# Optimization experiments

Hardware: AMD Instinct MI355X
Metric: run time of the kernel (lower is better)

## Reference

```python
import jax, jax.numpy as jnp
import numpy as np

B, N, H, L, V = 512, 24, 512, 64, 1024   # trees, nodes/tree, hidden, latent, vocab
MAX_NB = 8
T = 2 * (N - 1)      # DFS trace length per tree (each edge down + up)
PAD = T * B          # zero-padding slot in the message buffer


def _build_indices():
    rng = np.random.default_rng(0)
    wid = np.zeros((T, B), np.int32)
    ywid = np.zeros((T, B), np.int32)
    dirs = np.zeros((T, B), np.int32)
    hni = np.full((T, B, MAX_NB), PAD, np.int32)
    oni = np.full((T, B, MAX_NB), PAD, np.int32)
    rwid = np.zeros((B,), np.int32)
    roni = np.full((B, MAX_NB), PAD, np.int32)
    for b in range(B):
        deg = [0] * N
        nbr = [[] for _ in range(N)]
        for i in range(1, N):
            cand = [j for j in range(i) if deg[j] < MAX_NB]
            p = int(rng.choice(cand))
            nbr[p].append(i); nbr[i].append(p); deg[p] += 1; deg[i] += 1
        wids = rng.integers(0, V, N)
        trace = []
        def dfs(x, fa):
            for y in nbr[x]:
                if y == fa:
                    continue
                trace.append((x, y, 1)); dfs(y, x); trace.append((y, x, 0))
        dfs(0, -1)
        hkey = {}
        built = [[] for _ in range(N)]  # neighbors rebuilt as messages arrive
        for t, (x, y, d) in enumerate(trace):
            hn = [hkey[(z, x)] for z in built[x] if z != y]
            on = [hkey[(z, x)] for z in built[x]]
            hni[t, b, :len(hn)] = hn
            oni[t, b, :len(on)] = on
            wid[t, b] = wids[x]; ywid[t, b] = wids[y]; dirs[t, b] = d
            hkey[(x, y)] = t * B + b
            built[y].append(x)
        rwid[b] = wids[0]
        ron = [hkey[(z, 0)] for z in built[0]]
        roni[b, :len(ron)] = ron
    return wid, ywid, dirs, hni, oni, rwid, roni


def setup_inputs() -> dict:
    wid, ywid, dirs, hni, oni, rwid, roni = _build_indices()
    key = jax.random.key(0)
    ks = jax.random.split(key, 12)
    def pm(k, shape, s=0.05):
        return (jax.random.normal(k, shape) * s).astype(jnp.float32)
    return {
        "mol_vec": pm(ks[0], (B, L), 1.0),
        "wid": jnp.asarray(wid), "y_wid": jnp.asarray(ywid), "dirs": jnp.asarray(dirs),
        "h_nei_ids": jnp.asarray(hni), "o_nei_ids": jnp.asarray(oni),
        "root_wid": jnp.asarray(rwid), "root_o_nei_ids": jnp.asarray(roni),
        "emb": pm(ks[1], (V, H)),
        "Wz": pm(ks[2], (2 * H, H)), "bz": jnp.zeros((H,), jnp.float32),
        "Wr": pm(ks[3], (H, H)), "br": jnp.zeros((H,), jnp.float32),
        "Ur": pm(ks[4], (H, H)),
        "Wh": pm(ks[5], (2 * H, H)), "bh": jnp.zeros((H,), jnp.float32),
        "W": pm(ks[6], (L + H, H)), "bW": jnp.zeros((H,), jnp.float32),
        "U": pm(ks[7], (2 * H + L, H)), "bU": jnp.zeros((H,), jnp.float32),
        "Wo": pm(ks[8], (H, V)), "bo": jnp.zeros((V,), jnp.float32),
        "Us": pm(ks[9], (H, 1)), "bs": jnp.zeros((1,), jnp.float32),
    }


def _forward(mol_vec, emb, Wz, bz, Wr, br, Ur, Wh, bh, W, bW, U, bU, Wo, bo, Us, bs,
             wid, y_wid, dirs, h_nei_ids, o_nei_ids, root_wid, root_o_nei_ids):
    def gru(x, h_nei):  # x:[B,H], h_nei:[B,MAX_NB,H] (zero-padded)
        sum_h = h_nei.sum(1)
        z = jax.nn.sigmoid(jnp.concatenate([x, sum_h], -1) @ Wz + bz)
        r = jax.nn.sigmoid((x @ Wr + br)[:, None, :] + jnp.einsum('bnh,hk->bnk', h_nei, Ur))
        sum_g = (r * h_nei).sum(1)
        h_tilde = jnp.tanh(jnp.concatenate([x, sum_g], -1) @ Wh + bh)
        return (1.0 - z) * sum_h + z * h_tilde

    hbuf0 = jnp.zeros((T * B + 1, H), jnp.float32)  # last row = zero padding
    def step(hbuf, xs):
        t, w_t, ids_t = xs
        new_h = gru(emb[w_t], hbuf[ids_t])
        return jax.lax.dynamic_update_slice(hbuf, new_h, (t * B, 0)), None
    hbuf, _ = jax.lax.scan(step, hbuf0, (jnp.arange(T), wid, h_nei_ids))

    all_new_h = hbuf[:T * B]                  # [T*B, H] messages in step order
    cur_o = hbuf[o_nei_ids].sum(2)            # [T, B, H]
    x_emb = emb[wid]                          # [T, B, H]
    mv_rep = jnp.broadcast_to(mol_vec, (T, B, L))

    # ---- stop (BCE-with-logits, sum / B) ----
    stop_rows = jnp.concatenate([x_emb, cur_o, mv_rep], -1).reshape(T * B, 2 * H + L)
    root_row = jnp.concatenate([emb[root_wid], hbuf[root_o_nei_ids].sum(1), mol_vec], -1)
    stop_rows = jnp.concatenate([stop_rows, root_row], 0)
    stop_tgt = jnp.concatenate([dirs.reshape(-1).astype(jnp.float32), jnp.zeros((B,), jnp.float32)])
    s = (jax.nn.relu(stop_rows @ U + bU) @ Us + bs)[:, 0]
    stop_loss = (jnp.maximum(s, 0.0) - s * stop_tgt + jnp.log1p(jnp.exp(-jnp.abs(s)))).sum() / B
    stop_acc = jnp.mean(jnp.where((s >= 0.5) == (stop_tgt > 0.5), 1.0, 0.0))

    # ---- word prediction (CE, sum / B); root targets use zero hidden ----
    pred_h = jnp.concatenate([jnp.zeros((B, H), jnp.float32), all_new_h], 0)
    pred_mv = jnp.concatenate([mol_vec, mv_rep.reshape(T * B, L)], 0)
    pred_tgt = jnp.concatenate([root_wid, y_wid.reshape(-1)])
    mask = jnp.concatenate([jnp.ones((B,), jnp.float32), dirs.reshape(-1).astype(jnp.float32)])
    logits = jax.nn.relu(jnp.concatenate([pred_h, pred_mv], -1) @ W + bW) @ Wo + bo
    ls = jax.nn.log_softmax(logits, -1)
    ce = -jnp.take_along_axis(ls, pred_tgt[:, None], 1)[:, 0]
    pred_loss = (ce * mask).sum() / B
    preds = jnp.argmax(logits, 1)
    pred_acc = (jnp.where(preds == pred_tgt, 1.0, 0.0) * mask).sum() / mask.sum()
    return pred_loss, stop_loss, pred_acc, stop_acc


def reference(mol_vec, wid, y_wid, dirs, h_nei_ids, o_nei_ids, root_wid, root_o_nei_ids,
              emb, Wz, bz, Wr, br, Ur, Wh, bh, W, bW, U, bU, Wo, bo, Us, bs):
    return _forward(mol_vec, emb, Wz, bz, Wr, br, Ur, Wh, bh, W, bW, U, bU, Wo, bo, Us, bs,
                    wid, y_wid, dirs, h_nei_ids, o_nei_ids, root_wid, root_o_nei_ids)
```

## Files before the change

### kernel.cpp

```cpp
#include <hip/hip_runtime.h>
#include <hip/hip_bf16.h>

typedef __hip_bfloat16 bf16;
typedef __attribute__((ext_vector_type(8))) short bf16x8;
typedef __attribute__((ext_vector_type(4))) float f32x4;

static constexpr int Bb = 512;
static constexpr int Hh = 512;
static constexpr int Ll = 64;
static constexpr int Vv = 1024;
static constexpr int MAXNB = 8;
static constexpr int Tt = 46;
static constexpr int TB = Tt * Bb;
static constexpr int PADID = TB;
static constexpr int NROWS = TB + Bb;
static constexpr int XPS = 3 * Hh;

static constexpr int KU  = 2 * Hh + Ll;
static constexpr int KUP = KU + 8;
static constexpr int KW  = Hh + Ll;
static constexpr int KWP = KW + 8;
static constexpr int HP  = Hh + 8;

static constexpr int NT_U  = Hh / 16;
static constexpr int NT_WO = Vv / 16;

__device__ __forceinline__ float b2f(bf16 v) { return __bfloat162float(v); }
__device__ __forceinline__ float sigm(float x) { return 1.f / (1.f + __expf(-x)); }
__device__ __forceinline__ float bfu(unsigned short u) {
  return __uint_as_float((unsigned)u << 16);
}
__device__ __forceinline__ unsigned short f2bfu(float x) {
  bf16 v = __float2bfloat16(x);
  return *(unsigned short*)&v;
}

template <bool F32>
__device__ __forceinline__ float ldv(const void* p, long i) {
  if (F32) return ((const float*)p)[i];
  return __bfloat162float(((const bf16*)p)[i]);
}

__global__ void detect_kernel(const unsigned short* __restrict__ embu,
                              int* __restrict__ flag) {
  const long n = (long)Vv * Hh;
  int bad = 0;
  for (long i = blockIdx.x * 256 + threadIdx.x; i < n; i += 256L * 64) {
    unsigned short u = embu[i];
    if ((u & 0x7F80u) == 0x7F80u) bad = 1;
  }
  if (bad) atomicOr(flag, 1);
}

template <bool F32>
__device__ void xproj_body(const void* emb, const void* Wz, const void* bz,
                           const void* Wr, const void* br, const void* Wh,
                           const void* bh, bf16* xproj, float* xe) {
  const int v = blockIdx.x, k = threadIdx.x;
  xe[k] = ldv<F32>(emb, (long)v * Hh + k);
  __syncthreads();
  float z = ldv<F32>(bz, k);
  float r = ldv<F32>(br, k);
  float h = ldv<F32>(bh, k);
  for (int i = 0; i < Hh; ++i) {
    float a = xe[i];
    z += a * ldv<F32>(Wz, (long)i * Hh + k);
    r += a * ldv<F32>(Wr, (long)i * Hh + k);
    h += a * ldv<F32>(Wh, (long)i * Hh + k);
  }
  bf16* xp = xproj + (long)v * XPS;
  xp[k]          = __float2bfloat16(z);
  xp[Hh + k]     = __float2bfloat16(r);
  xp[2 * Hh + k] = __float2bfloat16(h);
}

__global__ __launch_bounds__(512) void xproj_kernel(
    const void* emb, const void* Wz, const void* bz, const void* Wr,
    const void* br, const void* Wh, const void* bh, bf16* xproj,
    const int* __restrict__ flag) {
  __shared__ float xe[Hh];
  if (*flag)
    xproj_body<true>(emb, Wz, bz, Wr, br, Wh, bh, xproj, xe);
  else
    xproj_body<false>(emb, Wz, bz, Wr, br, Wh, bh, xproj, xe);
}

template <bool F32>
__device__ __forceinline__ void wtt_body(const void* src, bf16* dst, int K,
                                         int N, int NT, int ro, int tk0,
                                         int tn0, unsigned short (*tile)[65]) {
  const int tid = threadIdx.x;
  const int ln = tid & 63;
  const int gr = tid >> 6;
  for (int kk = gr; kk < 64; kk += 4) {
    const int k = tk0 + kk, n = tn0 + ln;
    tile[ln][kk] = f2bfu(ldv<F32>(src, (long)(ro + k) * N + n));
  }
  __syncthreads();
  for (int nn = gr; nn < 64; nn += 4) {
    const int n = tn0 + nn, k = tk0 + ln;
    const long off = ((long)(k >> 5) * NT + (n >> 4)) * 512 +
                     ((k & 31) >> 3) * 128 + (n & 15) * 8 + (k & 7);
    dst[off] = *(bf16*)&tile[nn][ln];
  }
}

__global__ __launch_bounds__(256) void wt_kernel(
    const void* W, const void* U, const void* Wo, const void* Wz,
    const void* Ur, const void* Wh, bf16* wtW, bf16* wtU, bf16* wtWo,
    bf16* wgZ, bf16* wgR, bf16* wgH2, const int* __restrict__ flag) {
  __shared__ unsigned short tile[64][65];
  int b = blockIdx.x;
  const void* src; bf16* dst; int K, N, NT, ro, tk, tn;
  if (b < 72) {
    src = W; dst = wtW; K = KW; N = Hh; NT = NT_U; ro = 0; tk = b / 8; tn = b % 8;
  } else if (b < 208) {
    b -= 72; src = U; dst = wtU; K = KU; N = Hh; NT = NT_U; ro = 0; tk = b / 8; tn = b % 8;
  } else if (b < 336) {
    b -= 208; src = Wo; dst = wtWo; K = Hh; N = Vv; NT = NT_WO; ro = 0; tk = b / 16; tn = b % 16;
  } else if (b < 400) {
    b -= 336; src = Wz; dst = wgZ; K = Hh; N = Hh; NT = NT_U; ro = Hh; tk = b / 8; tn = b % 8;
  } else if (b < 464) {
    b -= 400; src = Ur; dst = wgR; K = Hh; N = Hh; NT = NT_U; ro = 0; tk = b / 8; tn = b % 8;
  } else {
    b -= 464; src = Wh; dst = wgH2; K = Hh; N = Hh; NT = NT_U; ro = Hh; tk = b / 8; tn = b % 8;
  }
  if (*flag) wtt_body<true>(src, dst, K, N, NT, ro, tk * 64, tn * 64, tile);
  else       wtt_body<false>(src, dst, K, N, NT, ro, tk * 64, tn * 64, tile);
}

__device__ __forceinline__ int gru_prep(int t, int b0, const int* hni,
                                        int* cid, int* rowf, int* nvs) {
  const int k = threadIdx.x;
  if (k < 2 * MAXNB)
    cid[k] = hni[((long)t * Bb + b0 + (k >> 3)) * MAXNB + (k & 7)];
  __syncthreads();
  if (k == 0) {
    int n0 = 0; while (n0 < MAXNB && cid[n0] != PADID) ++n0;
    int n1 = 0; while (n1 < MAXNB && cid[MAXNB + n1] != PADID) ++n1;
    for (int j = 0; j < n1; ++j) cid[n0 + j] = cid[MAXNB + j];
    for (int p = 0; p < n0 + n1; ++p) rowf[p] = (p >= n0) ? 1 : 0;
    nvs[0] = n0; nvs[1] = n1;
  }
  __syncthreads();
  return nvs[0] + nvs[1];
}

template <bool ABF, int S>
__device__ __forceinline__ void mfma_gemv(const bf16* __restrict__ Wt,
                                          const void* __restrict__ Abase,
                                          float* __restrict__ red,
                                          int wv, int l) {
  const int arow = l & 15;
  const int kofs = (l >> 4) * 8;
  f32x4 acc[4];
#pragma unroll
  for (int f = 0; f < 4; ++f) acc[f] = (f32x4){0.f, 0.f, 0.f, 0.f};

  for (int k0 = 0; k0 < Hh; k0 += 32) {
    unsigned short av[8] = {0, 0, 0, 0, 0, 0, 0, 0};
    if (arow < S) {
      if (ABF) {
        *(int4*)av = *(const int4*)((const bf16*)Abase + (long)arow * Hh +
                                    k0 + kofs);
      } else {
        const float* s = (const float*)Abase + (long)arow * Hh + k0 + kofs;
#pragma unroll
        for (int e = 0; e < 8; ++e) av[e] = f2bfu(s[e]);
      }
    }
    const bf16x8 a = *(const bf16x8*)av;
    const bf16* bkb = Wt + ((long)(k0 >> 5) * NT_U + wv * 4) * 512 + l * 8;
#pragma unroll
    for (int f = 0; f < 4; ++f) {
      const bf16x8 b = *(const bf16x8*)(bkb + f * 512);
      acc[f] = __builtin_amdgcn_mfma_f32_16x16x32_bf16(a, b, acc[f], 0, 0, 0);
    }
  }
#pragma unroll
  for (int f = 0; f < 4; ++f) {
    const int col = wv * 64 + f * 16 + (l & 15);
#pragma unroll
    for (int r = 0; r < 4; ++r) {
      const int row = (l >> 4) * 4 + r;
      if (row < S) red[row * Hh + col] = acc[f][r];
    }
  }
}

__global__ __launch_bounds__(512) void gru_step_xpb(
    int t, const int* __restrict__ wid, const int* __restrict__ hni,
    const bf16* __restrict__ xproj, const bf16* __restrict__ wgZ,
    const bf16* __restrict__ wgR, const bf16* __restrict__ wgH2,
    bf16* __restrict__ hbuf) {
  __shared__ float sh[2 * Hh];
  __shared__ float sg[2 * Hh];
  __shared__ __align__(16) unsigned short hnc[2 * MAXNB * Hh];
  __shared__ float red[4 * Hh];
  __shared__ int   cid[2 * MAXNB];
  __shared__ int   rowf[2 * MAXNB];
  __shared__ int   nvs[2];

  const int tid = threadIdx.x;
  const int k = tid;
  const int wv_ = tid >> 6;
  const int l = tid & 63;
  const int b0 = blockIdx.x * 2;
  const int P = gru_prep(t, b0, hni, cid, rowf, nvs);

  const int w0 = wid[t * Bb + b0];
  const int w1 = wid[t * Bb + b0 + 1];
  const bf16* xp0 = xproj + (long)w0 * XPS;
  const bf16* xp1 = xproj + (long)w1 * XPS;

  for (int p = wv_; p < P; p += 8) {
    const int4 d = *(const int4*)(hbuf + (long)cid[p] * Hh + 8 * l);
    *(int4*)(hnc + p * Hh + 8 * l) = d;
  }
  __syncthreads();

  float s0 = 0.f, s1 = 0.f;
  for (int p = 0; p < P; ++p) {
    const float hv = __bfloat162float(((const bf16*)hnc)[p * Hh + k]);
    if (rowf[p]) s1 += hv; else s0 += hv;
  }
  sh[k] = s0; sh[Hh + k] = s1;
  const float xz0 = b2f(xp0[k]),          xz1 = b2f(xp1[k]);
  const float xr0 = b2f(xp0[Hh + k]),     xr1 = b2f(xp1[Hh + k]);
  const float xh0 = b2f(xp0[2 * Hh + k]), xh1 = b2f(xp1[2 * Hh + k]);
  __syncthreads();

  mfma_gemv<false, 2>(wgZ, sh, red, wv_, l);
  __syncthreads();
  const float zp0 = xz0 + red[k];
  const float zp1 = xz1 + red[Hh + k];
  __syncthreads();

  float g0 = 0.f, g1 = 0.f;
  for (int c = 0; c < P; c += 4) {
    const int ns = (P - c >= 4) ? 4 : (P - c);
    const unsigned short* Ab = hnc + c * Hh;
    switch (ns) {
      case 1: mfma_gemv<true, 1>(wgR, Ab, red, wv_, l); break;
      case 2: mfma_gemv<true, 2>(wgR, Ab, red, wv_, l); break;
      case 3: mfma_gemv<true, 3>(wgR, Ab, red, wv_, l); break;
      default: mfma_gemv<true, 4>(wgR, Ab, red, wv_, l); break;
    }
    __syncthreads();
    for (int q = 0; q < ns; ++q) {
      const int p = c + q;
      const float rp = (rowf[p] ? xr1 : xr0) + red[q * Hh + k];
      const float cc =
          sigm(rp) * __bfloat162float(((const bf16*)hnc)[p * Hh + k]);
      if (rowf[p]) g1 += cc; else g0 += cc;
    }
    __syncthreads();
  }
  sg[k] = g0; sg[Hh + k] = g1;
  __syncthreads();

  mfma_gemv<false, 2>(wgH2, sg, red, wv_, l);
  __syncthreads();
  const float hp0 = xh0 + red[k];
  const float hp1 = xh1 + red[Hh + k];

  float z;
  z = sigm(zp0); const float o0 = (1.f - z) * s0 + z * tanhf(hp0);
  z = sigm(zp1); const float o1 = (1.f - z) * s1 + z * tanhf(hp1);
  hbuf[((long)t * Bb + b0) * Hh + k]     = __float2bfloat16(o0);
  hbuf[((long)t * Bb + b0 + 1) * Hh + k] = __float2bfloat16(o1);
}

template <bool F32, bool ABF, int S>
__device__ __forceinline__ void gemv_phase(const void* __restrict__ Wp,
                                           long wrow0,
                                           const void* __restrict__ Abase,
                                           float* __restrict__ red,
                                           int kg, int ch0) {
  float acc[S][4];
#pragma unroll
  for (int s = 0; s < S; ++s)
#pragma unroll
    for (int j = 0; j < 4; ++j) acc[s][j] = 0.f;
  const int i0 = kg * 128;
#pragma unroll 4
  for (int ii = 0; ii < 128; ++ii) {
    const int i = i0 + ii;
    float wv[4];
    if (F32) {
      const float4 f =
          *(const float4*)((const float*)Wp + (wrow0 + i) * (long)Hh + ch0);
      wv[0] = f.x; wv[1] = f.y; wv[2] = f.z; wv[3] = f.w;
    } else {
      const uint2 d =
          *(const uint2*)((const bf16*)Wp + (wrow0 + i) * (long)Hh + ch0);
      wv[0] = __uint_as_float(d.x << 16);
      wv[1] = __uint_as_float(d.x & 0xffff0000u);
      wv[2] = __uint_as_float(d.y << 16);
      wv[3] = __uint_as_float(d.y & 0xffff0000u);
    }
#pragma unroll
    for (int s = 0; s < S; ++s) {
      const float a = ABF
          ? __bfloat162float(((const bf16*)Abase)[s * Hh + i])
          : ((const float*)Abase)[s * Hh + i];
#pragma unroll
      for (int j = 0; j < 4; ++j) acc[s][j] += a * wv[j];
    }
  }
#pragma unroll
  for (int s = 0; s < S; ++s)
#pragma unroll
    for (int j = 0; j < 4; ++j)
      red[(kg * 4 + s) * Hh + ch0 + j] = acc[s][j];
}

template <bool F32>
__device__ void gru_body_xp(int t, const int* wid, const int* hni,
                            const bf16* xproj, const void* Wz, const void* Ur,
                            const void* Wh, bf16* hbuf, float* sh, float* sg,
                            unsigned short* hnc, float* red, int* cid,
                            int* rowf, int* nvs) {
  const int tid = threadIdx.x;
  const int k = tid;
  const int wv_ = tid >> 6;
  const int l = tid & 63;
  const int kg = wv_ >> 1;
  const int ch0 = (wv_ & 1) * 256 + l * 4;
  const int b0 = blockIdx.x * 2;
  const int P = gru_prep(t, b0, hni, cid, rowf, nvs);

  const int w0 = wid[t * Bb + b0];
  const int w1 = wid[t * Bb + b0 + 1];
  const bf16* xp0 = xproj + (long)w0 * XPS;
  const bf16* xp1 = xproj + (long)w1 * XPS;

  for (int p = wv_; p < P; p += 8) {
    const int4 d = *(const int4*)(hbuf + (long)cid[p] * Hh + 8 * l);
    *(int4*)(hnc + p * Hh + 8 * l) = d;
  }
  __syncthreads();

  float s0 = 0.f, s1 = 0.f;
  for (int p = 0; p < P; ++p) {
    const float hv = __bfloat162float(((const bf16*)hnc)[p * Hh + k]);
    if (rowf[p]) s1 += hv; else s0 += hv;
  }
  sh[k] = s0; sh[Hh + k] = s1;
  const float xz0 = b2f(xp0[k]),          xz1 = b2f(xp1[k]);
  const float xr0 = b2f(xp0[Hh + k]),     xr1 = b2f(xp1[Hh + k]);
  const float xh0 = b2f(xp0[2 * Hh + k]), xh1 = b2f(xp1[2 * Hh + k]);
  __syncthreads();

  gemv_phase<F32, false, 2>(Wz, Hh, sh, red, kg, ch0);
  __syncthreads();
  float zp0 = xz0, zp1 = xz1;
#pragma unroll
  for (int g = 0; g < 4; ++g) {
    zp0 += red[(g * 4 + 0) * Hh + k];
    zp1 += red[(g * 4 + 1) * Hh + k];
  }
  __syncthreads();

  float g0 = 0.f, g1 = 0.f;
  for (int c = 0; c < P; c += 4) {
    const int ns = (P - c >= 4) ? 4 : (P - c);
    const unsigned short* Ab = hnc + c * Hh;
    switch (ns) {
      case 1: gemv_phase<F32, true, 1>(Ur, 0, Ab, red, kg, ch0); break;
      case 2: gemv_phase<F32, true, 2>(Ur, 0, Ab, red, kg, ch0); break;
      case 3: gemv_phase<F32, true, 3>(Ur, 0, Ab, red, kg, ch0); break;
      default: gemv_phase<F32, true, 4>(Ur, 0, Ab, red, kg, ch0); break;
    }
    __syncthreads();
    for (int q = 0; q < ns; ++q) {
      const int p = c + q;
      float rp = rowf[p] ? xr1 : xr0;
#pragma unroll
      for (int g = 0; g < 4; ++g) rp += red[(g * 4 + q) * Hh + k];
      const float cc =
          sigm(rp) * __bfloat162float(((const bf16*)hnc)[p * Hh + k]);
      if (rowf[p]) g1 += cc; else g0 += cc;
    }
    __syncthreads();
  }
  sg[k] = g0; sg[Hh + k] = g1;
  __syncthreads();

  gemv_phase<F32, false, 2>(Wh, Hh, sg, red, kg, ch0);
  __syncthreads();
  float hp0 = xh0, hp1 = xh1;
#pragma unroll
  for (int g = 0; g < 4; ++g) {
    hp0 += red[(g * 4 + 0) * Hh + k];
    hp1 += red[(g * 4 + 1) * Hh + k];
  }

  float z;
  z = sigm(zp0); const float o0 = (1.f - z) * s0 + z * tanhf(hp0);
  z = sigm(zp1); const float o1 = (1.f - z) * s1 + z * tanhf(hp1);
  hbuf[((long)t * Bb + b0) * Hh + k]     = __float2bfloat16(o0);
  hbuf[((long)t * Bb + b0 + 1) * Hh + k] = __float2bfloat16(o1);
}

__global__ __launch_bounds__(512) void gru_step_xp(
    int t, const int* __restrict__ wid, const int* __restrict__ hni,
    const bf16* xproj, const void* Wz, const void* Ur, const void* Wh,
    bf16* hbuf, const int* __restrict__ flag) {
  __shared__ float sh[2 * Hh];
  __shared__ float sg[2 * Hh];
  __shared__ __align__(16) unsigned short hnc[2 * MAXNB * Hh];
  __shared__ float red[4 * 4 * Hh];
  __shared__ int   cid[2 * MAXNB];
  __shared__ int   rowf[2 * MAXNB];
  __shared__ int   nvs[2];
  if (*flag)
    gru_body_xp<true>(t, wid, hni, xproj, Wz, Ur, Wh, hbuf, sh, sg, hnc, red,
                      cid, rowf, nvs);
  else
    gru_body_xp<false>(t, wid, hni, xproj, Wz, Ur, Wh, hbuf, sh, sg, hnc, red,
                       cid, rowf, nvs);
}

template <bool F32, int P>
__device__ __forceinline__ void sumg(const void* Ur, int k, const float* hnc,
                                     float p0, float p1, const int* rowf,
                                     float& g0, float& g1) {
  float a[P];
#pragma unroll
  for (int p = 0; p < P; ++p) a[p] = rowf[p] ? p1 : p0;
  for (int i = 0; i < Hh; ++i) {
    float uv = ldv<F32>(Ur, (long)i * Hh + k);
#pragma unroll
    for (int p = 0; p < P; ++p) a[p] += hnc[p * Hh + i] * uv;
  }
#pragma unroll
  for (int p = 0; p < P; ++p) {
    float c = sigm(a[p]) * hnc[p * Hh + k];
    if (rowf[p]) g1 += c; else g0 += c;
  }
}

#define SUMG_SWITCH(F32V)                                                     \
  switch (P) {                                                                \
    case 1:  sumg<F32V, 1 >(Ur, k, hnc, p0, p1, rowf, g0, g1); break;         \
    case 2:  sumg<F32V, 2 >(Ur, k, hnc, p0, p1, rowf, g0, g1); break;         \
    case 3:  sumg<F32V, 3 >(Ur, k, hnc, p0, p1, rowf, g0, g1); break;         \
    case 4:  sumg<F32V, 4 >(Ur, k, hnc, p0, p1, rowf, g0, g1); break;         \
    case 5:  sumg<F32V, 5 >(Ur, k, hnc, p0, p1, rowf, g0, g1); break;         \
    case 6:  sumg<F32V, 6 >(Ur, k, hnc, p0, p1, rowf, g0, g1); break;         \
    case 7:  sumg<F32V, 7 >(Ur, k, hnc, p0, p1, rowf, g0, g1); break;         \
    case 8:  sumg<F32V, 8 >(Ur, k, hnc, p0, p1, rowf, g0, g1); break;         \
    case 9:  sumg<F32V, 9 >(Ur, k, hnc, p0, p1, rowf, g0, g1); break;         \
    case 10: sumg<F32V, 10>(Ur, k, hnc, p0, p1, rowf, g0, g1); break;         \
    case 11: sumg<F32V, 11>(Ur, k, hnc, p0, p1, rowf, g0, g1); break;         \
    case 12: sumg<F32V, 12>(Ur, k, hnc, p0, p1, rowf, g0, g1); break;         \
    case 13: sumg<F32V, 13>(Ur, k, hnc, p0, p1, rowf, g0, g1); break;         \
    case 14: sumg<F32V, 14>(Ur, k, hnc, p0, p1, rowf, g0, g1); break;         \
    case 15: sumg<F32V, 15>(Ur, k, hnc, p0, p1, rowf, g0, g1); break;         \
    case 16: sumg<F32V, 16>(Ur, k, hnc, p0, p1, rowf, g0, g1); break;         \
    default: break;                                                           \
  }

template <bool F32>
__device__ void gru_body(int t, const int* wid, const int* hni,
                         const void* emb, const void* Wz, const void* bz,
                         const void* Wr, const void* br, const void* Ur,
                         const void* Wh, const void* bh, bf16* hbuf,
                         float* xs, float* sh, float* sg, float* hnc,
                         int* cid, int* rowf, int* nvs) {
  const int k = threadIdx.x;
  const int b0 = blockIdx.x * 2;
  const int P = gru_prep(t, b0, hni, cid, rowf, nvs);

  const int w0 = wid[t * Bb + b0];
  const int w1 = wid[t * Bb + b0 + 1];
  xs[k]      = ldv<F32>(emb, (long)w0 * Hh + k);
  xs[Hh + k] = ldv<F32>(emb, (long)w1 * Hh + k);

  float s0 = 0.f, s1 = 0.f;
  for (int p = 0; p < P; ++p) {
    float hv = b2f(hbuf[(long)cid[p] * Hh + k]);
    hnc[p * Hh + k] = hv;
    if (rowf[p]) s1 += hv; else s0 += hv;
  }
  sh[k] = s0; sh[Hh + k] = s1;
  __syncthreads();

  float bzk = ldv<F32>(bz, k);
  float z0 = bzk, z1 = bzk;
  for (int i = 0; i < Hh; ++i) {
    float wv = ldv<F32>(Wz, (long)i * Hh + k);
    z0 += xs[i] * wv; z1 += xs[Hh + i] * wv;
  }
  for (int i = 0; i < Hh; ++i) {
    float wv = ldv<F32>(Wz, (long)(Hh + i) * Hh + k);
    z0 += sh[i] * wv; z1 += sh[Hh + i] * wv;
  }

  float brk = ldv<F32>(br, k);
  float p0 = brk, p1 = brk;
  for (int i = 0; i < Hh; ++i) {
    float wv = ldv<F32>(Wr, (long)i * Hh + k);
    p0 += xs[i] * wv; p1 += xs[Hh + i] * wv;
  }

  float g0 = 0.f, g1 = 0.f;
  SUMG_SWITCH(F32)
  sg[k] = g0; sg[Hh + k] = g1;
  __syncthreads();

  float bhk = ldv<F32>(bh, k);
  float h0 = bhk, h1 = bhk;
  for (int i = 0; i < Hh; ++i) {
    float wv = ldv<F32>(Wh, (long)i * Hh + k);
    h0 += xs[i] * wv; h1 += xs[Hh + i] * wv;
  }
  for (int i = 0; i < Hh; ++i) {
    float wv = ldv<F32>(Wh, (long)(Hh + i) * Hh + k);
    h0 += sg[i] * wv; h1 += sg[Hh + i] * wv;
  }

  float z;
  z = sigm(z0); float o0 = (1.f - z) * s0 + z * tanhf(h0);
  z = sigm(z1); float o1 = (1.f - z) * s1 + z * tanhf(h1);
  hbuf[((long)t * Bb + b0) * Hh + k]     = __float2bfloat16(o0);
  hbuf[((long)t * Bb + b0 + 1) * Hh + k] = __float2bfloat16(o1);
}

__global__ __launch_bounds__(512) void gru_step(
    int t, const int* __restrict__ wid, const int* __restrict__ hni,
    const void* emb, const void* Wz, const void* bz, const void* Wr,
    const void* br, const void* Ur, const void* Wh, const void* bh,
    bf16* hbuf, const int* __restrict__ flag) {
  __shared__ float xs[2 * Hh];
  __shared__ float sh[2 * Hh];
  __shared__ float sg[2 * Hh];
  __shared__ float hnc[2 * MAXNB * Hh];
  __shared__ int   cid[2 * MAXNB];
  __shared__ int   rowf[2 * MAXNB];
  __shared__ int   nvs[2];
  if (*flag)
    gru_body<true>(t, wid, hni, emb, Wz, bz, Wr, br, Ur, Wh, bh, hbuf,
                   xs, sh, sg, hnc, cid, rowf, nvs);
  else
    gru_body<false>(t, wid, hni, emb, Wz, bz, Wr, br, Ur, Wh, bh, hbuf,
                    xs, sh, sg, hnc, cid, rowf, nvs);
}

template <bool F32>
__device__ void stop_mfma_body(
    const void* mol_vec, const int* wid, const int* dirs, const int* oni,
    const int* root_wid, const int* roni, const void* emb,
    const bf16* __restrict__ wtU, const void* bU, const void* Us,
    const void* bs, const bf16* __restrict__ hbuf, float* accum,
    unsigned short* As, float* bU_l, float* Us_l, int* wl, int* bl,
    float* tgl, int* idsl, float* sred) {
  const int tid = threadIdx.x;
  const int l = tid & 63, w = tid >> 6;
  const int r0 = blockIdx.x * 16;

  bU_l[tid] = ldv<F32>(bU, tid);
  bU_l[tid + 256] = ldv<F32>(bU, tid + 256);
  Us_l[tid] = ldv<F32>(Us, tid);
  Us_l[tid + 256] = ldv<F32>(Us, tid + 256);
  if (tid < 16) {
    const int gi = r0 + tid;
    if (gi < TB) { wl[tid] = wid[gi]; bl[tid] = gi % Bb; tgl[tid] = (float)dirs[gi]; }
    else { const int j = gi - TB; wl[tid] = root_wid[j]; bl[tid] = j; tgl[tid] = 0.f; }
  }
  if (tid < 128) {
    const int rr = tid >> 3, jj = tid & 7;
    const int gi = r0 + rr;
// ... 316 lines not shown
__global__ __launch_bounds__(256) void pred_mfma(
    const void* mol_vec, const int* __restrict__ y_wid,
    const int* __restrict__ dirs, const int* __restrict__ root_wid,
    const bf16* __restrict__ wtW, const void* bW,
    const bf16* __restrict__ wtWo, const void* bo,
    const bf16* __restrict__ hbuf, float* accum,
    const int* __restrict__ flag) {
  __shared__ __align__(16) unsigned short As1[16 * KWP];
  __shared__ __align__(16) unsigned short hidl[16 * HP];
  __shared__ float bW_l[Hh];
  __shared__ float bo_l[Vv];
  __shared__ float maxw[16 * 4];
  __shared__ int   idxw[16 * 4];
  __shared__ float sumw[16 * 4];
  __shared__ float gmaxl[16];
  __shared__ int   gidxl[16];
  __shared__ float sbl[16];
  __shared__ int   tgtl[16];
  __shared__ float mskl[16];
  if (*flag)
    pred_mfma_body<true>(mol_vec, y_wid, dirs, root_wid, wtW, bW, wtWo, bo,
                         hbuf, accum, As1, hidl, bW_l, bo_l, maxw, idxw, sumw,
                         gmaxl, gidxl, sbl, tgtl, mskl);
  else
    pred_mfma_body<false>(mol_vec, y_wid, dirs, root_wid, wtW, bW, wtWo, bo,
                          hbuf, accum, As1, hidl, bW_l, bo_l, maxw, idxw,
                          sumw, gmaxl, gidxl, sbl, tgtl, mskl);
}

template <bool F32>
__device__ void stop_body(const void* mol_vec, const int* wid,
                          const int* dirs, const int* oni,
                          const int* root_wid, const int* roni,
                          const void* emb, const void* U, const void* bU,
                          const void* Us, const void* bs, const bf16* hbuf,
                          float* accum,
                          float (*srow)[2 * Hh + Ll], float (*red)[256],
                          float* fin) {
  const int tid = threadIdx.x;
  const int i0 = blockIdx.x * 8;
  const int K = 2 * Hh + Ll;

  for (int r = 0; r < 8; ++r) {
    int i = i0 + r;
    int w, b;
    const int* ids;
    if (i < TB) { w = wid[i]; b = i % Bb; ids = &oni[(long)i * MAXNB]; }
    else { int j = i - TB; w = root_wid[j]; b = j; ids = &roni[(long)j * MAXNB]; }
    for (int c = tid; c < K; c += 256) {
      float v;
      if (c < Hh) v = ldv<F32>(emb, (long)w * Hh + c);
      else if (c < 2 * Hh) {
        int cc = c - Hh;
        float s = 0.f;
        for (int j = 0; j < MAXNB; ++j) s += b2f(hbuf[(long)ids[j] * Hh + cc]);
        v = s;
      } else v = ldv<F32>(mol_vec, (long)b * Ll + (c - 2 * Hh));
      srow[r][c] = v;
    }
  }
  __syncthreads();

  const int k0 = tid, k1 = tid + 256;
  float acc[8][2] = {};
  for (int kk = 0; kk < K; ++kk) {
    float u0 = ldv<F32>(U, (long)kk * Hh + k0);
    float u1 = ldv<F32>(U, (long)kk * Hh + k1);
#pragma unroll
    for (int r = 0; r < 8; ++r) {
      float a = srow[r][kk];
      acc[r][0] += a * u0; acc[r][1] += a * u1;
    }
  }
  float bU0 = ldv<F32>(bU, k0), bU1 = ldv<F32>(bU, k1);
  float us0 = ldv<F32>(Us, k0), us1 = ldv<F32>(Us, k1);
  __syncthreads();
#pragma unroll
  for (int r = 0; r < 8; ++r)
    red[r][tid] = fmaxf(acc[r][0] + bU0, 0.f) * us0 + fmaxf(acc[r][1] + bU1, 0.f) * us1;
  __syncthreads();
  for (int off = 128; off; off >>= 1) {
    if (tid < off) {
#pragma unroll
      for (int r = 0; r < 8; ++r) red[r][tid] += red[r][tid + off];
    }
    __syncthreads();
  }
  if (tid < 8) {
    int i = i0 + tid;
    float s = red[tid][0] + ldv<F32>(bs, 0);
    float tgt = (i < TB) ? (float)dirs[i] : 0.f;
    float loss = fmaxf(s, 0.f) - s * tgt + log1pf(expf(-fabsf(s)));
    float ok = ((s >= 0.5f) == (tgt > 0.5f)) ? 1.f : 0.f;
    fin[tid] = loss; fin[8 + tid] = ok;
  }
  __syncthreads();
  if (tid == 0) {
    float ls = 0.f, oks = 0.f;
    for (int r = 0; r < 8; ++r) { ls += fin[r]; oks += fin[8 + r]; }
    atomicAdd(&accum[0], ls);
    atomicAdd(&accum[1], oks);
  }
}

__global__ __launch_bounds__(256) void stop_kernel(
    const void* mol_vec, const int* __restrict__ wid,
    const int* __restrict__ dirs, const int* __restrict__ oni,
    const int* __restrict__ root_wid, const int* __restrict__ roni,
    const void* emb, const void* U, const void* bU, const void* Us,
    const void* bs, const bf16* hbuf, float* accum,
    const int* __restrict__ flag) {
  __shared__ float srow[8][2 * Hh + Ll];
  __shared__ float red[8][256];
  __shared__ float fin[16];
  if (*flag)
    stop_body<true>(mol_vec, wid, dirs, oni, root_wid, roni, emb, U, bU, Us,
                    bs, hbuf, accum, srow, red, fin);
  else
    stop_body<false>(mol_vec, wid, dirs, oni, root_wid, roni, emb, U, bU, Us,
                     bs, hbuf, accum, srow, red, fin);
}

template <bool F32>
__device__ void pred_body(const void* mol_vec, const int* y_wid,
                          const int* dirs, const int* root_wid, const void* W,
                          const void* bW, const void* Wo, const void* bo,
                          const bf16* hbuf, float* accum,
                          float (*srow)[Hh + Ll], float (*hid)[Hh],
                          float* rv, int* ri, float* sb) {
  const int tid = threadIdx.x;
  const int i0 = blockIdx.x * 8;
  const int K1 = Hh + Ll;

  for (int r = 0; r < 8; ++r) {
    int i = i0 + r;
    int b = (i < Bb) ? i : (i - Bb) % Bb;
    for (int c = tid; c < K1; c += 256) {
      float v;
      if (c < Hh) v = (i < Bb) ? 0.f : b2f(hbuf[(long)(i - Bb) * Hh + c]);
      else v = ldv<F32>(mol_vec, (long)b * Ll + (c - Hh));
      srow[r][c] = v;
    }
  }
  __syncthreads();

  const int k0 = tid, k1 = tid + 256;
  float acc[8][2] = {};
  for (int kk = 0; kk < K1; ++kk) {
    float w0 = ldv<F32>(W, (long)kk * Hh + k0);
    float w1 = ldv<F32>(W, (long)kk * Hh + k1);
#pragma unroll
    for (int r = 0; r < 8; ++r) {
      float a = srow[r][kk];
      acc[r][0] += a * w0; acc[r][1] += a * w1;
    }
  }
  float bW0 = ldv<F32>(bW, k0), bW1 = ldv<F32>(bW, k1);
#pragma unroll
  for (int r = 0; r < 8; ++r) {
    hid[r][k0] = fmaxf(acc[r][0] + bW0, 0.f);
    hid[r][k1] = fmaxf(acc[r][1] + bW1, 0.f);
  }
  __syncthreads();

  float lg[8][4] = {};
  for (int kk = 0; kk < Hh; ++kk) {
    float w0 = ldv<F32>(Wo, (long)kk * Vv + tid);
    float w1 = ldv<F32>(Wo, (long)kk * Vv + tid + 256);
    float w2 = ldv<F32>(Wo, (long)kk * Vv + tid + 512);
    float w3 = ldv<F32>(Wo, (long)kk * Vv + tid + 768);
#pragma unroll
    for (int r = 0; r < 8; ++r) {
      float a = hid[r][kk];
      lg[r][0] += a * w0; lg[r][1] += a * w1;
      lg[r][2] += a * w2; lg[r][3] += a * w3;
    }
  }
  float bo0 = ldv<F32>(bo, tid);
  float bo1 = ldv<F32>(bo, tid + 256);
  float bo2 = ldv<F32>(bo, tid + 512);
  float bo3 = ldv<F32>(bo, tid + 768);

  float plloss = 0.f, pnum = 0.f, pmask = 0.f;
  for (int r = 0; r < 8; ++r) {
    int i = i0 + r;
    int tgt = (i < Bb) ? root_wid[i] : y_wid[i - Bb];
    float msk = (i < Bb) ? 1.f : (float)dirs[i - Bb];
    float v0 = lg[r][0] + bo0, v1 = lg[r][1] + bo1;
    float v2 = lg[r][2] + bo2, v3 = lg[r][3] + bo3;

    float bm = v0; int bi = tid;
    if (v1 > bm) { bm = v1; bi = tid + 256; }
    if (v2 > bm) { bm = v2; bi = tid + 512; }
    if (v3 > bm) { bm = v3; bi = tid + 768; }
    rv[tid] = bm; ri[tid] = bi;
    if ((tgt & 255) == tid) {
      int cc = tgt >> 8;
      sb[0] = (cc == 0) ? v0 : (cc == 1) ? v1 : (cc == 2) ? v2 : v3;
    }
    __syncthreads();
    for (int off = 128; off; off >>= 1) {
      if (tid < off) {
        float o = rv[tid + off]; int oi = ri[tid + off];
        if (o > rv[tid] || (o == rv[tid] && oi < ri[tid])) { rv[tid] = o; ri[tid] = oi; }
      }
      __syncthreads();
    }
    float m = rv[0];
    int am = ri[0];
    __syncthreads();
    rv[tid] = __expf(v0 - m) + __expf(v1 - m) + __expf(v2 - m) + __expf(v3 - m);
    __syncthreads();
    for (int off = 128; off; off >>= 1) {
      if (tid < off) rv[tid] += rv[tid + off];
      __syncthreads();
    }
    if (tid == 0) {
      float lse = m + __logf(rv[0]);
      float ce = lse - sb[0];
      plloss += ce * msk;
      pnum += (am == tgt) ? msk : 0.f;
      pmask += msk;
    }
    __syncthreads();
  }
  if (tid == 0) {
    atomicAdd(&accum[2], plloss);
    atomicAdd(&accum[3], pnum);
    atomicAdd(&accum[4], pmask);
  }
}

__global__ __launch_bounds__(256) void pred_kernel(
    const void* mol_vec, const int* __restrict__ y_wid,
    const int* __restrict__ dirs, const int* __restrict__ root_wid,
    const void* W, const void* bW, const void* Wo, const void* bo,
    const bf16* hbuf, float* accum, const int* __restrict__ flag) {
  __shared__ float srow[8][Hh + Ll];
  __shared__ float hid[8][Hh];
  __shared__ float rv[256];
  __shared__ int   ri[256];
  __shared__ float sb[2];
  if (*flag)
    pred_body<true>(mol_vec, y_wid, dirs, root_wid, W, bW, Wo, bo, hbuf,
                    accum, srow, hid, rv, ri, sb);
  else
    pred_body<false>(mol_vec, y_wid, dirs, root_wid, W, bW, Wo, bo, hbuf,
                     accum, srow, hid, rv, ri, sb);
}

__global__ void finalize_kernel(const float* __restrict__ accum,
                                const int* __restrict__ flag, void* out) {
  if (threadIdx.x == 0 && blockIdx.x == 0) {
    float o0 = accum[2] / (float)Bb;
    float o1 = accum[0] / (float)Bb;
    float o2 = accum[3] / accum[4];
    float o3 = accum[1] / (float)NROWS;
    if (*flag) {
      float* o = (float*)out;
      o[0] = o0; o[1] = o1; o[2] = o2; o[3] = o3;
    } else {
      bf16* o = (bf16*)out;
      o[0] = __float2bfloat16(o0); o[1] = __float2bfloat16(o1);
      o[2] = __float2bfloat16(o2); o[3] = __float2bfloat16(o3);
    }
  }
}

extern "C" void kernel_launch(void* const* d_in, const int* in_sizes, int n_in,
                              void* d_out, int out_size, void* d_ws, size_t ws_size,
                              hipStream_t stream) {
  const void* mol_vec  = d_in[0];
  const int*  wid      = (const int*)d_in[1];
  const int*  y_wid    = (const int*)d_in[2];
  const int*  dirs     = (const int*)d_in[3];
  const int*  hni      = (const int*)d_in[4];
  const int*  oni      = (const int*)d_in[5];
  const int*  root_wid = (const int*)d_in[6];
  const int*  roni     = (const int*)d_in[7];
  const void* emb      = d_in[8];
  const void* Wz       = d_in[9];
  const void* bz       = d_in[10];
  const void* Wr       = d_in[11];
  const void* br       = d_in[12];
  const void* Ur       = d_in[13];
  const void* Wh       = d_in[14];
  const void* bh       = d_in[15];
  const void* W        = d_in[16];
  const void* bW       = d_in[17];
  const void* U        = d_in[18];
  const void* bU       = d_in[19];
  const void* Wo       = d_in[20];
  const void* bo       = d_in[21];
  const void* Us       = d_in[22];
  const void* bs       = d_in[23];

  float* accum = (float*)d_ws;
  int*   flag  = (int*)d_ws + 8;
  bf16*  hbuf  = (bf16*)((char*)d_ws + 64);
  bf16*  xproj = hbuf + (long)(TB + 1) * Hh;
  bf16*  wtW   = xproj + (long)Vv * XPS;
  bf16*  wtU   = wtW + (long)Hh * KW;
  bf16*  wtWo  = wtU + (long)Hh * KU;
  bf16*  wgZ   = wtWo + (long)Vv * Hh;
  bf16*  wgR   = wgZ + (long)Hh * Hh;
  bf16*  wgH2  = wgR + (long)Hh * Hh;

  const size_t need_xp = 64 + ((size_t)(TB + 1) * Hh + (size_t)Vv * XPS) * sizeof(bf16);
  const size_t need_m  = need_xp +
      ((size_t)Hh * KW + (size_t)Hh * KU + (size_t)Vv * Hh) * sizeof(bf16);
  const size_t need_g  = need_m + 3ull * Hh * Hh * sizeof(bf16);
  const bool use_xp = (ws_size >= need_xp);
  const bool useM   = (ws_size >= need_m);
  const bool useG   = (ws_size >= need_g);

  hipMemsetAsync(d_ws, 0, 64, stream);
  hipMemsetAsync(hbuf + (long)TB * Hh, 0, Hh * sizeof(bf16), stream);

  detect_kernel<<<64, 256, 0, stream>>>((const unsigned short*)emb, flag);

  if (useM) {
    const int nblk = useG ? 528 : 336;
    wt_kernel<<<nblk, 256, 0, stream>>>(W, U, Wo, Wz, Ur, Wh, wtW, wtU, wtWo,
                                        wgZ, wgR, wgH2, flag);
  }
  if (use_xp) {
    xproj_kernel<<<Vv, 512, 0, stream>>>(emb, Wz, bz, Wr, br, Wh, bh, xproj, flag);
    if (useG) {
      for (int t = 0; t < Tt; ++t) {
        gru_step_xpb<<<Bb / 2, 512, 0, stream>>>(t, wid, hni, xproj, wgZ, wgR,
                                                 wgH2, hbuf);
      }
    } else {
      for (int t = 0; t < Tt; ++t) {
        gru_step_xp<<<Bb / 2, 512, 0, stream>>>(t, wid, hni, xproj, Wz, Ur,
                                                Wh, hbuf, flag);
      }
    }
  } else {
    for (int t = 0; t < Tt; ++t) {
      gru_step<<<Bb / 2, 512, 0, stream>>>(t, wid, hni, emb, Wz, bz, Wr, br,
                                           Ur, Wh, bh, hbuf, flag);
    }
  }

  if (useM) {
    stop_mfma<<<NROWS / 16, 256, 0, stream>>>(mol_vec, wid, dirs, oni,
                                              root_wid, roni, emb, wtU, bU, Us,
                                              bs, hbuf, accum, flag);
    pred_mfma<<<NROWS / 16, 256, 0, stream>>>(mol_vec, y_wid, dirs, root_wid,
                                              wtW, bW, wtWo, bo, hbuf, accum,
                                              flag);
  } else {
    stop_kernel<<<NROWS / 8, 256, 0, stream>>>(mol_vec, wid, dirs, oni,
                                               root_wid, roni, emb, U, bU, Us,
                                               bs, hbuf, accum, flag);
    pred_kernel<<<NROWS / 8, 256, 0, stream>>>(mol_vec, y_wid, dirs, root_wid,
                                               W, bW, Wo, bo, hbuf, accum,
                                               flag);
  }
  finalize_kernel<<<1, 64, 0, stream>>>(accum, flag, d_out);
}
```

Measured before the change: 1.771 ms.

## Fuse z-gate and r-gate GEMVs into one concatenated MFMA pass

```diff
diff --git a/kernel.cpp b/kernel.cpp
--- a/kernel.cpp
+++ b/kernel.cpp
@@ -87,8 +87,9 @@
 
 template <bool F32>
 __device__ __forceinline__ void wtt_body(const void* src, bf16* dst, int K,
-                                         int N, int NT, int ro, int tk0,
-                                         int tn0, unsigned short (*tile)[65]) {
+                                         int N, int NT, int ro, int co,
+                                         int tk0, int tn0,
+                                         unsigned short (*tile)[65]) {
   const int tid = threadIdx.x;
   const int ln = tid & 63;
   const int gr = tid >> 6;
@@ -98,7 +99,7 @@
   }
   __syncthreads();
   for (int nn = gr; nn < 64; nn += 4) {
-    const int n = tn0 + nn, k = tk0 + ln;
+    const int n = tn0 + nn + co, k = tk0 + ln;
     const long off = ((long)(k >> 5) * NT + (n >> 4)) * 512 +
                      ((k & 31) >> 3) * 128 + (n & 15) * 8 + (k & 7);
     dst[off] = *(bf16*)&tile[nn][ln];
@@ -108,25 +109,25 @@
 __global__ __launch_bounds__(256) void wt_kernel(
     const void* W, const void* U, const void* Wo, const void* Wz,
     const void* Ur, const void* Wh, bf16* wtW, bf16* wtU, bf16* wtWo,
-    bf16* wgZ, bf16* wgR, bf16* wgH2, const int* __restrict__ flag) {
+    bf16* wgZR, bf16* wgH2, const int* __restrict__ flag) {
   __shared__ unsigned short tile[64][65];
   int b = blockIdx.x;
-  const void* src; bf16* dst; int K, N, NT, ro, tk, tn;
+  const void* src; bf16* dst; int K, N, NT, ro, co, tk, tn;
   if (b < 72) {
-    src = W; dst = wtW; K = KW; N = Hh; NT = NT_U; ro = 0; tk = b / 8; tn = b % 8;
+    src = W; dst = wtW; K = KW; N = Hh; NT = NT_U; ro = 0; co = 0; tk = b / 8; tn = b % 8;
   } else if (b < 208) {
-    b -= 72; src = U; dst = wtU; K = KU; N = Hh; NT = NT_U; ro = 0; tk = b / 8; tn = b % 8;
+    b -= 72; src = U; dst = wtU; K = KU; N = Hh; NT = NT_U; ro = 0; co = 0; tk = b / 8; tn = b % 8;
   } else if (b < 336) {
-    b -= 208; src = Wo; dst = wtWo; K = Hh; N = Vv; NT = NT_WO; ro = 0; tk = b / 16; tn = b % 16;
+    b -= 208; src = Wo; dst = wtWo; K = Hh; N = Vv; NT = NT_WO; ro = 0; co = 0; tk = b / 16; tn = b % 16;
   } else if (b < 400) {
-    b -= 336; src = Wz; dst = wgZ; K = Hh; N = Hh; NT = NT_U; ro = Hh; tk = b / 8; tn = b % 8;
+    b -= 336; src = Wz; dst = wgZR; K = Hh; N = Hh; NT = NT_WO; ro = Hh; co = 0; tk = b / 8; tn = b % 8;
   } else if (b < 464) {
-    b -= 400; src = Ur; dst = wgR; K = Hh; N = Hh; NT = NT_U; ro = 0; tk = b / 8; tn = b % 8;
+    b -= 400; src = Ur; dst = wgZR; K = Hh; N = Hh; NT = NT_WO; ro = 0; co = 512; tk = b / 8; tn = b % 8;
   } else {
-    b -= 464; src = Wh; dst = wgH2; K = Hh; N = Hh; NT = NT_U; ro = Hh; tk = b / 8; tn = b % 8;
-  }
-  if (*flag) wtt_body<true>(src, dst, K, N, NT, ro, tk * 64, tn * 64, tile);
-  else       wtt_body<false>(src, dst, K, N, NT, ro, tk * 64, tn * 64, tile);
+    b -= 464; src = Wh; dst = wgH2; K = Hh; N = Hh; NT = NT_U; ro = Hh; co = 0; tk = b / 8; tn = b % 8;
+  }
+  if (*flag) wtt_body<true>(src, dst, K, N, NT, ro, co, tk * 64, tn * 64, tile);
+  else       wtt_body<false>(src, dst, K, N, NT, ro, co, tk * 64, tn * 64, tile);
 }
 
 __device__ __forceinline__ int gru_prep(int t, int b0, const int* hni,
@@ -144,6 +145,49 @@
   }
   __syncthreads();
   return nvs[0] + nvs[1];
+}
+
+__device__ __forceinline__ void mfma_gemv_zr(
+    const bf16* __restrict__ Wt, const float* __restrict__ sh,
+    const unsigned short* __restrict__ hnc, int pbase, int np,
+    float* __restrict__ red, int wv, int l) {
+  const int arow = l & 15;
+  const int kofs = (l >> 4) * 8;
+  f32x4 acc[8];
+#pragma unroll
+  for (int f = 0; f < 8; ++f) acc[f] = (f32x4){0.f, 0.f, 0.f, 0.f};
+
+  for (int k0 = 0; k0 < Hh; k0 += 32) {
+    unsigned short av[8] = {0, 0, 0, 0, 0, 0, 0, 0};
+    if (arow < 2) {
+      const float* s = sh + (long)arow * Hh + k0 + kofs;
+#pragma unroll
+      for (int e = 0; e < 8; ++e) av[e] = f2bfu(s[e]);
+    } else if (arow - 2 < np) {
+      *(int4*)av = *(const int4*)(hnc + (long)(pbase + arow - 2) * Hh +
+                                  k0 + kofs);
+    }
+    const bf16x8 a = *(const bf16x8*)av;
+    const bf16* bkb = Wt + ((long)(k0 >> 5) * NT_WO + wv * 8) * 512 + l * 8;
+#pragma unroll
+    for (int f = 0; f < 8; ++f) {
+      const bf16x8 b = *(const bf16x8*)(bkb + f * 512);
+      acc[f] = __builtin_amdgcn_mfma_f32_16x16x32_bf16(a, b, acc[f], 0, 0, 0);
+    }
+  }
+#pragma unroll
+  for (int f = 0; f < 8; ++f) {
+    const int col = wv * 128 + f * 16 + (l & 15);
+#pragma unroll
+    for (int r = 0; r < 4; ++r) {
+      const int row = (l >> 4) * 4 + r;
+      if (col < 512) {
+        if (row < 2) red[row * Hh + col] = acc[f][r];
+      } else if (row >= 2) {
+        red[row * Hh + (col - 512)] = acc[f][r];
+      }
+    }
+  }
 }
 
 template <bool ABF, int S>
@@ -190,13 +234,12 @@
 
 __global__ __launch_bounds__(512) void gru_step_xpb(
     int t, const int* __restrict__ wid, const int* __restrict__ hni,
-    const bf16* __restrict__ xproj, const bf16* __restrict__ wgZ,
-    const bf16* __restrict__ wgR, const bf16* __restrict__ wgH2,
-    bf16* __restrict__ hbuf) {
+    const bf16* __restrict__ xproj, const bf16* __restrict__ wgZR,
+    const bf16* __restrict__ wgH2, bf16* __restrict__ hbuf) {
   __shared__ float sh[2 * Hh];
   __shared__ float sg[2 * Hh];
   __shared__ __align__(16) unsigned short hnc[2 * MAXNB * Hh];
-  __shared__ float red[4 * Hh];
+  __shared__ float red[16 * Hh];
   __shared__ int   cid[2 * MAXNB];
   __shared__ int   rowf[2 * MAXNB];
   __shared__ int   nvs[2];
@@ -230,32 +273,28 @@
   const float xh0 = b2f(xp0[2 * Hh + k]), xh1 = b2f(xp1[2 * Hh + k]);
   __syncthreads();
 
-  mfma_gemv<false, 2>(wgZ, sh, red, wv_, l);
-  __syncthreads();
-  const float zp0 = xz0 + red[k];
-  const float zp1 = xz1 + red[Hh + k];
-  __syncthreads();
-
   float g0 = 0.f, g1 = 0.f;
-  for (int c = 0; c < P; c += 4) {
-    const int ns = (P - c >= 4) ? 4 : (P - c);
-    const unsigned short* Ab = hnc + c * Hh;
-    switch (ns) {
-      case 1: mfma_gemv<true, 1>(wgR, Ab, red, wv_, l); break;
-      case 2: mfma_gemv<true, 2>(wgR, Ab, red, wv_, l); break;
-      case 3: mfma_gemv<true, 3>(wgR, Ab, red, wv_, l); break;
-      default: mfma_gemv<true, 4>(wgR, Ab, red, wv_, l); break;
-    }
+  float zp0 = 0.f, zp1 = 0.f;
+  int c0 = 0;
+  do {
+    int np = P - c0;
+    if (np > 14) np = 14;
+    if (np < 0) np = 0;
+    mfma_gemv_zr(wgZR, sh, hnc, c0, np, red, wv_, l);
     __syncthreads();
-    for (int q = 0; q < ns; ++q) {
-      const int p = c + q;
-      const float rp = (rowf[p] ? xr1 : xr0) + red[q * Hh + k];
-      const float cc =
-          sigm(rp) * __bfloat162float(((const bf16*)hnc)[p * Hh + k]);
+    if (c0 == 0) {
+      zp0 = xz0 + red[k];
+      zp1 = xz1 + red[Hh + k];
+    }
+    for (int q = 0; q < np; ++q) {
+      const int p = c0 + q;
+      const float rp = (rowf[p] ? xr1 : xr0) + red[(2 + q) * Hh + k];
+      const float cc = sigm(rp) * bfu(hnc[p * Hh + k]);
       if (rowf[p]) g1 += cc; else g0 += cc;
     }
     __syncthreads();
-  }
+    c0 += 14;
+  } while (c0 < P);
   sg[k] = g0; sg[Hh + k] = g1;
   __syncthreads();
 
@@ -1191,14 +1230,14 @@
   bf16*  wtW   = xproj + (long)Vv * XPS;
   bf16*  wtU   = wtW + (long)Hh * KW;
   bf16*  wtWo  = wtU + (long)Hh * KU;
-  bf16*  wgZ   = wtWo + (long)Vv * Hh;
-  bf16*  wgR   = wgZ + (long)Hh * Hh;
-  bf16*  wgH2  = wgR + (long)Hh * Hh;
+  bf16*  wgZR  = wtWo + (long)Vv * Hh;
+  bf16*  wgH2  = wgZR + (long)Hh * Vv;
 
   const size_t need_xp = 64 + ((size_t)(TB + 1) * Hh + (size_t)Vv * XPS) * sizeof(bf16);
   const size_t need_m  = need_xp +
       ((size_t)Hh * KW + (size_t)Hh * KU + (size_t)Vv * Hh) * sizeof(bf16);
-  const size_t need_g  = need_m + 3ull * Hh * Hh * sizeof(bf16);
+  const size_t need_g  = need_m +
+      ((size_t)Hh * Vv + (size_t)Hh * Hh) * sizeof(bf16);
   const bool use_xp = (ws_size >= need_xp);
   const bool useM   = (ws_size >= need_m);
   const bool useG   = (ws_size >= need_g);
@@ -1211,13 +1250,13 @@
   if (useM) {
     const int nblk = useG ? 528 : 336;
     wt_kernel<<<nblk, 256, 0, stream>>>(W, U, Wo, Wz, Ur, Wh, wtW, wtU, wtWo,
-                                        wgZ, wgR, wgH2, flag);
+                                        wgZR, wgH2, flag);
   }
   if (use_xp) {
     xproj_kernel<<<Vv, 512, 0, stream>>>(emb, Wz, bz, Wr, br, Wh, bh, xproj, flag);
     if (useG) {
       for (int t = 0; t < Tt; ++t) {
-        gru_step_xpb<<<Bb / 2, 512, 0, stream>>>(t, wid, hni, xproj, wgZ, wgR,
+        gru_step_xpb<<<Bb / 2, 512, 0, stream>>>(t, wid, hni, xproj, wgZR,
                                                  wgH2, hbuf);
       }
     } else {
```

New measurement: 4.355 ms. 146% more time.

## Process four trees per GRU step block to reuse weight loads

Applied to the files above, without the earlier changes.

```diff
diff --git a/kernel.cpp b/kernel.cpp
--- a/kernel.cpp
+++ b/kernel.cpp
@@ -146,6 +146,26 @@
   return nvs[0] + nvs[1];
 }
 
+__device__ __forceinline__ int gru_prep4(int t, int b0, const int* hni,
+                                         int* cid, int* rowf, int* nvs) {
+  const int k = threadIdx.x;
+  if (k < 4 * MAXNB)
+    cid[32 + k] = hni[((long)t * Bb + b0 + (k >> 3)) * MAXNB + (k & 7)];
+  __syncthreads();
+  if (k == 0) {
+    int P = 0;
+    for (int m = 0; m < 4; ++m)
+      for (int j = 0; j < MAXNB; ++j) {
+        const int v = cid[32 + m * MAXNB + j];
+        if (v == PADID) break;
+        cid[P] = v; rowf[P] = m; ++P;
+      }
+    nvs[0] = P;
+  }
+  __syncthreads();
+  return nvs[0];
+}
+
 template <bool ABF, int S>
 __device__ __forceinline__ void mfma_gemv(const bf16* __restrict__ Wt,
                                           const void* __restrict__ Abase,
@@ -193,25 +213,25 @@
     const bf16* __restrict__ xproj, const bf16* __restrict__ wgZ,
     const bf16* __restrict__ wgR, const bf16* __restrict__ wgH2,
     bf16* __restrict__ hbuf) {
-  __shared__ float sh[2 * Hh];
-  __shared__ float sg[2 * Hh];
-  __shared__ __align__(16) unsigned short hnc[2 * MAXNB * Hh];
+  __shared__ float sh[4 * Hh];
+  __shared__ float sg[4 * Hh];
+  __shared__ __align__(16) unsigned short hnc[4 * MAXNB * Hh];
   __shared__ float red[4 * Hh];
-  __shared__ int   cid[2 * MAXNB];
-  __shared__ int   rowf[2 * MAXNB];
+  __shared__ int   cid[64];
+  __shared__ int   rowf[4 * MAXNB];
   __shared__ int   nvs[2];
 
   const int tid = threadIdx.x;
   const int k = tid;
   const int wv_ = tid >> 6;
   const int l = tid & 63;
-  const int b0 = blockIdx.x * 2;
-  const int P = gru_prep(t, b0, hni, cid, rowf, nvs);
-
-  const int w0 = wid[t * Bb + b0];
-  const int w1 = wid[t * Bb + b0 + 1];
-  const bf16* xp0 = xproj + (long)w0 * XPS;
-  const bf16* xp1 = xproj + (long)w1 * XPS;
+  const int b0 = blockIdx.x * 4;
+  const int P = gru_prep4(t, b0, hni, cid, rowf, nvs);
+
+  const bf16* xp0 = xproj + (long)wid[t * Bb + b0] * XPS;
+  const bf16* xp1 = xproj + (long)wid[t * Bb + b0 + 1] * XPS;
+  const bf16* xp2 = xproj + (long)wid[t * Bb + b0 + 2] * XPS;
+  const bf16* xp3 = xproj + (long)wid[t * Bb + b0 + 3] * XPS;
 
   for (int p = wv_; p < P; p += 8) {
     const int4 d = *(const int4*)(hbuf + (long)cid[p] * Hh + 8 * l);
@@ -219,24 +239,31 @@
   }
   __syncthreads();
 
-  float s0 = 0.f, s1 = 0.f;
+  float s0 = 0.f, s1 = 0.f, s2 = 0.f, s3 = 0.f;
   for (int p = 0; p < P; ++p) {
-    const float hv = __bfloat162float(((const bf16*)hnc)[p * Hh + k]);
-    if (rowf[p]) s1 += hv; else s0 += hv;
-  }
-  sh[k] = s0; sh[Hh + k] = s1;
+    const float hv = bfu(hnc[p * Hh + k]);
+    const int m = rowf[p];
+    if (m == 0) s0 += hv; else if (m == 1) s1 += hv;
+    else if (m == 2) s2 += hv; else s3 += hv;
+  }
+  sh[k] = s0; sh[Hh + k] = s1; sh[2 * Hh + k] = s2; sh[3 * Hh + k] = s3;
   const float xz0 = b2f(xp0[k]),          xz1 = b2f(xp1[k]);
+  const float xz2 = b2f(xp2[k]),          xz3 = b2f(xp3[k]);
   const float xr0 = b2f(xp0[Hh + k]),     xr1 = b2f(xp1[Hh + k]);
+  const float xr2 = b2f(xp2[Hh + k]),     xr3 = b2f(xp3[Hh + k]);
   const float xh0 = b2f(xp0[2 * Hh + k]), xh1 = b2f(xp1[2 * Hh + k]);
-  __syncthreads();
-
-  mfma_gemv<false, 2>(wgZ, sh, red, wv_, l);
+  const float xh2 = b2f(xp2[2 * Hh + k]), xh3 = b2f(xp3[2 * Hh + k]);
+  __syncthreads();
+
+  mfma_gemv<false, 4>(wgZ, sh, red, wv_, l);
   __syncthreads();
   const float zp0 = xz0 + red[k];
   const float zp1 = xz1 + red[Hh + k];
-  __syncthreads();
-
-  float g0 = 0.f, g1 = 0.f;
+  const float zp2 = xz2 + red[2 * Hh + k];
+  const float zp3 = xz3 + red[3 * Hh + k];
+  __syncthreads();
+
+  float g0 = 0.f, g1 = 0.f, g2 = 0.f, g3 = 0.f;
   for (int c = 0; c < P; c += 4) {
     const int ns = (P - c >= 4) ? 4 : (P - c);
     const unsigned short* Ab = hnc + c * Hh;
@@ -249,26 +276,33 @@
     __syncthreads();
     for (int q = 0; q < ns; ++q) {
       const int p = c + q;
-      const float rp = (rowf[p] ? xr1 : xr0) + red[q * Hh + k];
-      const float cc =
-          sigm(rp) * __bfloat162float(((const bf16*)hnc)[p * Hh + k]);
-      if (rowf[p]) g1 += cc; else g0 += cc;
+      const int m = rowf[p];
+      const float xrm = (m == 0) ? xr0 : (m == 1) ? xr1 : (m == 2) ? xr2 : xr3;
+      const float cc = sigm(xrm + red[q * Hh + k]) * bfu(hnc[p * Hh + k]);
+      if (m == 0) g0 += cc; else if (m == 1) g1 += cc;
+      else if (m == 2) g2 += cc; else g3 += cc;
     }
     __syncthreads();
   }
-  sg[k] = g0; sg[Hh + k] = g1;
-  __syncthreads();
-
-  mfma_gemv<false, 2>(wgH2, sg, red, wv_, l);
+  sg[k] = g0; sg[Hh + k] = g1; sg[2 * Hh + k] = g2; sg[3 * Hh + k] = g3;
+  __syncthreads();
+
+  mfma_gemv<false, 4>(wgH2, sg, red, wv_, l);
   __syncthreads();
   const float hp0 = xh0 + red[k];
   const float hp1 = xh1 + red[Hh + k];
+  const float hp2 = xh2 + red[2 * Hh + k];
+  const float hp3 = xh3 + red[3 * Hh + k];
 
   float z;
   z = sigm(zp0); const float o0 = (1.f - z) * s0 + z * tanhf(hp0);
   z = sigm(zp1); const float o1 = (1.f - z) * s1 + z * tanhf(hp1);
+  z = sigm(zp2); const float o2 = (1.f - z) * s2 + z * tanhf(hp2);
+  z = sigm(zp3); const float o3 = (1.f - z) * s3 + z * tanhf(hp3);
   hbuf[((long)t * Bb + b0) * Hh + k]     = __float2bfloat16(o0);
   hbuf[((long)t * Bb + b0 + 1) * Hh + k] = __float2bfloat16(o1);
+  hbuf[((long)t * Bb + b0 + 2) * Hh + k] = __float2bfloat16(o2);
+  hbuf[((long)t * Bb + b0 + 3) * Hh + k] = __float2bfloat16(o3);
 }
 
 template <bool F32, bool ABF, int S>
@@ -1217,7 +1251,7 @@
     xproj_kernel<<<Vv, 512, 0, stream>>>(emb, Wz, bz, Wr, br, Wh, bh, xproj, flag);
     if (useG) {
       for (int t = 0; t < Tt; ++t) {
-        gru_step_xpb<<<Bb / 2, 512, 0, stream>>>(t, wid, hni, xproj, wgZ, wgR,
+        gru_step_xpb<<<Bb / 4, 512, 0, stream>>>(t, wid, hni, xproj, wgZ, wgR,
                                                  wgH2, hbuf);
       }
     } else {
```

Result: slower. 2.095 ms (+18.3%).
